# Kernel optimization log

Measured on AMD Instinct MI355X. Metric: run time of the kernel, lower is better.

The kernel has to match this reference:

```python
import jax, jax.numpy as jnp
import numpy as np

B, S, D, H = 2, 2048, 1024, 16
HD = D // H
SCALE = HD ** -0.5

def setup_inputs() -> dict:
    key = jax.random.key(0)
    ks = jax.random.split(key, 5)
    x = jax.random.normal(ks[0], (B, S, D), dtype=jnp.float32)
    Wqkv = jax.random.normal(ks[1], (D, 3 * D), dtype=jnp.float32) * (D ** -0.5)
    bqkv = jnp.zeros((3 * D,), dtype=jnp.float32)
    Wproj = jax.random.normal(ks[2], (D, D), dtype=jnp.float32) * (D ** -0.5)
    bproj = jnp.zeros((D,), dtype=jnp.float32)
    return {"x": x, "Wqkv": Wqkv, "bqkv": bqkv, "Wproj": Wproj, "bproj": bproj}

def reference(x, Wqkv, bqkv, Wproj, bproj):
    b, s, _ = x.shape
    qkv = x @ Wqkv + bqkv                       # [B,S,3D]
    qkv = qkv.reshape(b, s, 3, H, HD)
    q, k, v = [jnp.transpose(qkv[:, :, i], (0, 2, 1, 3)) for i in range(3)]  # [B,H,S,HD]
    attn = jnp.einsum('bhqd,bhkd->bhqk', q, k) * SCALE   # [B,H,S,S]
    attn = jax.nn.softmax(attn, axis=-1)
    out = jnp.einsum('bhqk,bhkd->bhqd', attn, v)         # [B,H,S,HD]
    out = jnp.transpose(out, (0, 2, 1, 3)).reshape(b, s, D)
    return out @ Wproj + bproj
```

## Files before the change

### kernel.cpp

```cpp
#include <hip/hip_runtime.h>
#include <hip/hip_bf16.h>

#define BB 2
#define SS 2048
#define DD 1024
#define HH 16
#define HDD 64
#define MM (BB*SS)
#define NQKV (3*DD)
#define SCALE 0.125f
#define QPRESCALE 0.18033688f

typedef __bf16 bf16_t;
typedef bf16_t bf16x4 __attribute__((ext_vector_type(4)));
typedef bf16_t bf16x8 __attribute__((ext_vector_type(8)));
typedef float f32x4 __attribute__((ext_vector_type(4)));
typedef float f32x16 __attribute__((ext_vector_type(16)));

__device__ __forceinline__ void gl_lds16(const bf16_t* g, bf16_t* l) {
    __builtin_amdgcn_global_load_lds(
        (const __attribute__((address_space(1))) unsigned int*)(uintptr_t)g,
        (__attribute__((address_space(3))) unsigned int*)(uintptr_t)l,
        16, 0, 0);
}

__device__ __forceinline__ f32x4 MF(bf16x8 a, bf16x8 b, f32x4 c) {
    return __builtin_amdgcn_mfma_f32_16x16x32_bf16(a, b, c, 0, 0, 0);
}

__global__ __launch_bounds__(256) void prep(
    const float* __restrict__ x, const float* __restrict__ Wqkv,
    const float* __restrict__ Wproj, bf16_t* __restrict__ xb,
    bf16_t* __restrict__ wqkvt, bf16_t* __restrict__ wprojt)
{
    const int bx = blockIdx.x;
    if (bx < 2048) {
        int i = (bx * 256 + threadIdx.x) * 8;
        float4 a = *(const float4*)(x + i);
        float4 b = *(const float4*)(x + i + 4);
        bf16x8 v;
        v[0]=(bf16_t)a.x; v[1]=(bf16_t)a.y; v[2]=(bf16_t)a.z; v[3]=(bf16_t)a.w;
        v[4]=(bf16_t)b.x; v[5]=(bf16_t)b.y; v[6]=(bf16_t)b.z; v[7]=(bf16_t)b.w;
        *reinterpret_cast<bf16x8*>(xb + i) = v;
        return;
    }
    __shared__ float tile[32][33];
    const float* src; bf16_t* dst; int C, bxl, byl;
    if (bx < 5120) {
        int t = bx - 2048;
        byl = t / 96; bxl = t - byl * 96;
        src = Wqkv;  dst = wqkvt;  C = NQKV;
    } else {
        int t = bx - 5120;
        byl = t >> 5; bxl = t & 31;
        src = Wproj; dst = wprojt; C = DD;
    }
    const int R = DD;
    const int tx = threadIdx.x & 31, ty = threadIdx.x >> 5;
    const int r0 = byl * 32, c0 = bxl * 32;
    #pragma unroll
    for (int i = 0; i < 32; i += 8)
        tile[ty + i][tx] = src[(size_t)(r0 + ty + i) * C + c0 + tx];
    __syncthreads();
    #pragma unroll
    for (int i = 0; i < 32; i += 8)
        dst[(size_t)(c0 + ty + i) * R + r0 + tx] = (bf16_t)tile[tx][ty + i];
}

__global__ __launch_bounds__(512, 2) void gemm_qkv(
    const bf16_t* __restrict__ A, const bf16_t* __restrict__ Bt,
    const float* __restrict__ bias,
    bf16_t* __restrict__ qw, bf16_t* __restrict__ kw, bf16_t* __restrict__ vtw)
{
    constexpr int K  = DD;
    constexpr int BM = 256, BN = 192, BK = 32;
    constexpr int NT = K / BK;

    __shared__ __align__(16) bf16_t smem[50176];
    bf16_t* const Ab[3] = { smem, smem + 8192, smem + 16384 };
    bf16_t* const Bb[3] = { smem + 24576, smem + 30720, smem + 36864 };

    const int tid  = threadIdx.x;
    const int w    = tid >> 6;
    const int lane = tid & 63;
    const int lr   = lane & 15;
    const int quad = lane >> 4;
    const int wm   = w >> 2;
    const int wn   = w & 3;

    const int flat = blockIdx.y * 16 + blockIdx.x;
    const int swz  = (flat & 7) * 32 + (flat >> 3);
    const int m0   = (swz >> 4) * BM;
    const int n0   = (swz & 15) * BN;

    f32x4 acc[8][3];
    #pragma unroll
    for (int mi = 0; mi < 8; mi++)
        #pragma unroll
        for (int ni = 0; ni < 3; ni++)
            acc[mi][ni] = (f32x4){0.f, 0.f, 0.f, 0.f};

    const int ca0 = tid,        ca1 = tid + 512;
    const int cb0 = tid,        cb1 = tid + 256;
    const bf16_t* aG0 = A  + (size_t)(m0 + (ca0 >> 2)) * K + (ca0 & 3) * 8;
    const bf16_t* aG1 = A  + (size_t)(m0 + (ca1 >> 2)) * K + (ca1 & 3) * 8;
    const bf16_t* bG0 = Bt + (size_t)(n0 + (cb0 >> 2)) * K + (cb0 & 3) * 8;
    const bf16_t* bG1 = Bt + (size_t)(n0 + (cb1 >> 2)) * K + (cb1 & 3) * 8;

    auto stage = [&](int kt, bf16_t* Ad, bf16_t* Bd) {
        const int ko = kt * BK;
        gl_lds16(aG0 + ko, Ad + ca0 * 8);
        gl_lds16(aG1 + ko, Ad + ca1 * 8);
        gl_lds16(bG0 + ko, Bd + cb0 * 8);
        gl_lds16(bG1 + ko, Bd + cb1 * 8);
    };

    stage(0, Ab[0], Bb[0]);
    stage(1, Ab[1], Bb[1]);
    asm volatile("s_waitcnt vmcnt(4)" ::: "memory");
    __builtin_amdgcn_s_barrier();
    __builtin_amdgcn_sched_barrier(0);

    const int aOff = (wm * 128 + lr) * BK + quad * 8;
    const int bOff = (wn * 48  + lr) * BK + quad * 8;

    auto tileStep = [&](int t, const bf16_t* Ac, const bf16_t* Bc,
                        bf16_t* An, bf16_t* Bn) {
        bf16x8 af[8], bk[3];
        #pragma unroll
        for (int mi = 0; mi < 8; mi++)
            af[mi] = *(const bf16x8*)(Ac + aOff + mi * 16 * BK);
        #pragma unroll
        for (int ni = 0; ni < 3; ni++)
            bk[ni] = *(const bf16x8*)(Bc + bOff + ni * 16 * BK);
        if (t < NT - 2) stage(t + 2, An, Bn);
        __builtin_amdgcn_sched_barrier(0);
        __builtin_amdgcn_s_setprio(1);
        #pragma unroll
        for (int mi = 0; mi < 8; mi++)
            #pragma unroll
            for (int ni = 0; ni < 3; ni++)
                acc[mi][ni] = MF(af[mi], bk[ni], acc[mi][ni]);
        __builtin_amdgcn_s_setprio(0);
        __builtin_amdgcn_sched_barrier(0);
        if (t < NT - 2)       asm volatile("s_waitcnt vmcnt(4)" ::: "memory");
        else if (t == NT - 2) asm volatile("s_waitcnt vmcnt(0)" ::: "memory");
        __builtin_amdgcn_s_barrier();
        __builtin_amdgcn_sched_barrier(0);
    };

    #pragma unroll 1
    for (int tt = 0; tt < NT - 2; tt += 3) {
        tileStep(tt,     Ab[0], Bb[0], Ab[2], Bb[2]);
        tileStep(tt + 1, Ab[1], Bb[1], Ab[0], Bb[0]);
        tileStep(tt + 2, Ab[2], Bb[2], Ab[1], Bb[1]);
    }
    tileStep(NT - 2, Ab[0], Bb[0], nullptr, nullptr);
    tileStep(NT - 1, Ab[1], Bb[1], nullptr, nullptr);

    __builtin_amdgcn_s_barrier();

    const int colBase = n0 + wn * 48;
    const int vbase   = (n0 < 2048) ? 2048 : n0;
    #pragma unroll
    for (int mi = 0; mi < 8; mi++) {
        const int rl0 = wm * 128 + mi * 16 + quad * 4;
        #pragma unroll
        for (int ni = 0; ni < 3; ni++) {
            const int col = colBase + ni * 16 + lr;
            const float bcol = bias[col];
            const int which = col >> 10;
            const int d = col & 1023;
            const int h = d >> 6, hd = d & 63;
            if (which == 0) {
                #pragma unroll
                for (int reg = 0; reg < 4; reg++) {
                    const int row = m0 + rl0 + reg;
                    const int b = row >> 11, s = row & 2047;
                    qw[(((size_t)(b * HH + h)) * SS + s) * HDD + hd] =
                        (bf16_t)((acc[mi][ni][reg] + bcol) * QPRESCALE);
                }
            } else if (which == 1) {
                #pragma unroll
                for (int reg = 0; reg < 4; reg++) {
                    const int row = m0 + rl0 + reg;
                    const int b = row >> 11, s = row & 2047;
                    kw[(((size_t)(b * HH + h)) * SS + s) * HDD + hd] =
                        (bf16_t)(acc[mi][ni][reg] + bcol);
                }
            } else {
                bf16x4 pk;
                #pragma unroll
                for (int reg = 0; reg < 4; reg++)
                    pk[reg] = (bf16_t)(acc[mi][ni][reg] + bcol);
                const int lc = col - vbase;
                *reinterpret_cast<bf16x4*>(&smem[lc * 260 + rl0]) = pk;
            }
        }
    }
    const int nv = n0 + BN - 2048;
    if (nv > 0) {
        __builtin_amdgcn_s_barrier();
        const int nvc = nv < BN ? nv : BN;
        const int lcb = tid >> 5;
        const int rl  = (tid & 31) * 8;
        const int b   = m0 >> 11;
        const int s   = (m0 & 2047) + rl;
        for (int j = 0; j < nvc / 16; j++) {
            const int lc = j * 16 + lcb;
            bf16x8 vv = *reinterpret_cast<const bf16x8*>(&smem[lc * 260 + rl]);
            const int col = vbase + lc;
            const int d = col & 1023;
            const int h = d >> 6, hd = d & 63;
            *reinterpret_cast<bf16x8*>(
                vtw + (((size_t)(b * HH + h)) * HDD + hd) * SS + s) = vv;
        }
    }
}

__global__ __launch_bounds__(512, 6) void gemm_proj(
    const bf16_t* __restrict__ A, const bf16_t* __restrict__ Bt,
    const float* __restrict__ bias, float* __restrict__ outf)
{
    constexpr int K  = DD;
    constexpr int N  = DD;
    constexpr int BM = 128, BN = 128, BK = 32;
    constexpr int NT = K / BK;

    __shared__ __align__(16) bf16_t smem[24576];
    bf16_t* const Ab[3] = { smem, smem + 4096, smem + 8192 };
    bf16_t* const Bb[3] = { smem + 12288, smem + 16384, smem + 20480 };

    const int tid  = threadIdx.x;
    const int w    = tid >> 6;
    const int lane = tid & 63;
    const int lr   = lane & 15;
    const int quad = lane >> 4;
    const int wm   = w >> 2;
    const int wn   = w & 3;

    const int flat = blockIdx.y * 8 + blockIdx.x;
    const int swz  = (flat & 7) * 32 + (flat >> 3);
    const int m0   = (swz >> 3) * BM;
    const int n0   = (swz & 7) * BN;

    f32x4 acc[4][2];
    #pragma unroll
    for (int mi = 0; mi < 4; mi++)
        #pragma unroll
        for (int ni = 0; ni < 2; ni++)
            acc[mi][ni] = (f32x4){0.f, 0.f, 0.f, 0.f};

    const bf16_t* aG = A  + (size_t)(m0 + (tid >> 2)) * K + (tid & 3) * 8;
    const bf16_t* bG = Bt + (size_t)(n0 + (tid >> 2)) * K + (tid & 3) * 8;

    auto stage = [&](int kt, bf16_t* Ad, bf16_t* Bd) {
        const int ko = kt * BK;
        gl_lds16(aG + ko, Ad + tid * 8);
        gl_lds16(bG + ko, Bd + tid * 8);
    };

    stage(0, Ab[0], Bb[0]);
    stage(1, Ab[1], Bb[1]);
    asm volatile("s_waitcnt vmcnt(2)" ::: "memory");
    __builtin_amdgcn_s_barrier();
    __builtin_amdgcn_sched_barrier(0);

    const int aOff = (wm * 64 + lr) * BK + quad * 8;
    const int bOff = (wn * 32 + lr) * BK + quad * 8;

    auto tileStep = [&](int t, const bf16_t* Ac, const bf16_t* Bc,
                        bf16_t* An, bf16_t* Bn) {
        bf16x8 af[4], bk[2];
        #pragma unroll
        for (int mi = 0; mi < 4; mi++)
            af[mi] = *(const bf16x8*)(Ac + aOff + mi * 16 * BK);
        #pragma unroll
        for (int ni = 0; ni < 2; ni++)
            bk[ni] = *(const bf16x8*)(Bc + bOff + ni * 16 * BK);
        if (t < NT - 2) stage(t + 2, An, Bn);
        __builtin_amdgcn_sched_barrier(0);
        __builtin_amdgcn_s_setprio(1);
        #pragma unroll
        for (int mi = 0; mi < 4; mi++)
            #pragma unroll
            for (int ni = 0; ni < 2; ni++)
                acc[mi][ni] = MF(af[mi], bk[ni], acc[mi][ni]);
        __builtin_amdgcn_s_setprio(0);
        __builtin_amdgcn_sched_barrier(0);
        if (t < NT - 2)       asm volatile("s_waitcnt vmcnt(2)" ::: "memory");
        else if (t == NT - 2) asm volatile("s_waitcnt vmcnt(0)" ::: "memory");
        __builtin_amdgcn_s_barrier();
        __builtin_amdgcn_sched_barrier(0);
    };

    #pragma unroll 1
    for (int tt = 0; tt < NT - 2; tt += 3) {
        tileStep(tt,     Ab[0], Bb[0], Ab[2], Bb[2]);
        tileStep(tt + 1, Ab[1], Bb[1], Ab[0], Bb[0]);
        tileStep(tt + 2, Ab[2], Bb[2], Ab[1], Bb[1]);
    }
    tileStep(NT - 2, Ab[0], Bb[0], nullptr, nullptr);
    tileStep(NT - 1, Ab[1], Bb[1], nullptr, nullptr);

    #pragma unroll
    for (int mi = 0; mi < 4; mi++)
        #pragma unroll
        for (int ni = 0; ni < 2; ni++) {
            const int col = n0 + wn * 32 + ni * 16 + lr;
            const float bcol = bias[col];
            #pragma unroll
            for (int reg = 0; reg < 4; reg++) {
                const int row = m0 + wm * 64 + mi * 16 + quad * 4 + reg;
                outf[(size_t)row * N + col] = acc[mi][ni][reg] + bcol;
            }
        }
}

__global__ __launch_bounds__(512, 4) void attn_kernel(
    const bf16_t* __restrict__ qws, const bf16_t* __restrict__ kws,
    const bf16_t* __restrict__ vtws, bf16_t* __restrict__ ob)
{
    __shared__ __align__(16) bf16_t smem[35072];
    bf16_t* Ks = smem;
    bf16_t* Vs = smem + 16640;

    const int tid  = threadIdx.x;
    const int w    = tid >> 6;
    const int g    = w >> 2;
    const int wg   = w & 3;
    const int lane = tid & 63;
    const int ln31 = lane & 31;
    const int ln5  = lane >> 5;

    const int flat = blockIdx.y * 16 + blockIdx.x;
    const int t2 = flat >> 3;
    const int bh = (t2 >> 4) * 8 + (flat & 7);
    const int qb = t2 & 15;
    const int b  = bh >> 4;
    const int h  = bh & 15;

    const bf16_t* Qh  = qws  + (size_t)bh * SS * HDD;
    const bf16_t* Kh  = kws  + (size_t)bh * SS * HDD;
    const bf16_t* Vth = vtws + (size_t)bh * HDD * SS;

    const int q0w    = qb * 128 + wg * 32;
    const int kvbase = g * 1024;

    bf16x8 aq[4];
    #pragma unroll
    for (int f = 0; f < 4; f++)
        aq[f] = *(const bf16x8*)(Qh + (size_t)(q0w + ln31) * HDD + f * 16 + ln5 * 8);

    const int gtid = tid & 255;
    const int sc = gtid & 7;
    const int sr = gtid >> 3;
    const int vcol = (sc >> 1) * 16 + (sc & 1) * 4;

    {
        const int ko = g * 520;
        const int vo = g * 4608;
        bf16x8 k0 = *(const bf16x8*)(Kh  + (size_t)(kvbase + sr     ) * HDD + sc * 8);
        bf16x8 k1 = *(const bf16x8*)(Kh  + (size_t)(kvbase + sr + 32) * HDD + sc * 8);
        bf16x8 v0 = *(const bf16x8*)(Vth + (size_t)(sr     ) * SS + kvbase + sc * 8);
        bf16x8 v1 = *(const bf16x8*)(Vth + (size_t)(sr + 32) * SS + kvbase + sc * 8);
        *reinterpret_cast<bf16x8*>(&Ks[(ko + sc * 65 + sr     ) * 8]) = k0;
        *reinterpret_cast<bf16x8*>(&Ks[(ko + sc * 65 + sr + 32) * 8]) = k1;
        bf16_t* vd0 = &Vs[vo + (sr     ) * 72 + vcol];
        bf16_t* vd1 = &Vs[vo + (sr + 32) * 72 + vcol];
        *reinterpret_cast<bf16x4*>(vd0)     = __builtin_shufflevector(v0, v0, 0,1,2,3);
        *reinterpret_cast<bf16x4*>(vd0 + 8) = __builtin_shufflevector(v0, v0, 4,5,6,7);
        *reinterpret_cast<bf16x4*>(vd1)     = __builtin_shufflevector(v1, v1, 0,1,2,3);
        *reinterpret_cast<bf16x4*>(vd1 + 8) = __builtin_shufflevector(v1, v1, 4,5,6,7);
    }
    __syncthreads();

    float l = 0.f;
    f32x16 o[2];
    #pragma unroll
    for (int nh = 0; nh < 2; nh++)
        #pragma unroll
        for (int r = 0; r < 16; r++) o[nh][r] = 0.f;

    int buf = 0;
    for (int it = 0; it < 16; ++it) {
        const int ko = buf * 1040 + g * 520;
        const int vo = buf * 9216 + g * 4608;

        bf16x8 nk0, nk1, nv0, nv1;
        const bool more = (it + 1 < 16);
        if (more) {
            const int kvn = kvbase + (it + 1) * 64;
            nk0 = *(const bf16x8*)(Kh  + (size_t)(kvn + sr     ) * HDD + sc * 8);
            nk1 = *(const bf16x8*)(Kh  + (size_t)(kvn + sr + 32) * HDD + sc * 8);
            nv0 = *(const bf16x8*)(Vth + (size_t)(sr     ) * SS + kvn + sc * 8);
            nv1 = *(const bf16x8*)(Vth + (size_t)(sr + 32) * SS + kvn + sc * 8);
        }

        f32x16 sfr[2];
        __builtin_amdgcn_s_setprio(1);
        #pragma unroll
        for (int ni = 0; ni < 2; ni++) {
            #pragma unroll
            for (int r = 0; r < 16; r++) sfr[ni][r] = 0.f;
            #pragma unroll
            for (int f = 0; f < 4; f++) {
                bf16x8 kb = *reinterpret_cast<const bf16x8*>(
                    &Ks[(ko + (2 * f + ln5) * 65 + ni * 32 + ln31) * 8]);
                sfr[ni] = __builtin_amdgcn_mfma_f32_32x32x16_bf16(kb, aq[f], sfr[ni], 0, 0, 0);
            }
        }
        __builtin_amdgcn_s_setprio(0);

        float p[2][16];
        #pragma unroll
        for (int ni = 0; ni < 2; ni++)
            #pragma unroll
            for (int r = 0; r < 16; r++) {
                p[ni][r] = __builtin_amdgcn_exp2f(sfr[ni][r]);
                l += p[ni][r];
            }

        bf16x8 ap[4];
        #pragma unroll
        for (int c16 = 0; c16 < 4; c16++)
            #pragma unroll
            for (int j = 0; j < 8; j++)
                ap[c16][j] = (bf16_t)p[c16 >> 1][(c16 & 1) * 8 + j];

        __builtin_amdgcn_s_setprio(1);
        #pragma unroll
        for (int nh = 0; nh < 2; nh++) {
            const bf16_t* vrow = &Vs[vo + (nh * 32 + ln31) * 72];
            #pragma unroll
            for (int c16 = 0; c16 < 4; c16++) {
                bf16x8 vb = *reinterpret_cast<const bf16x8*>(vrow + c16 * 16 + 8 * ln5);
                o[nh] = __builtin_amdgcn_mfma_f32_32x32x16_bf16(ap[c16], vb, o[nh], 0, 0, 0);
            }
        }
        __builtin_amdgcn_s_setprio(0);

        if (more) {
            const int ko1 = (buf ^ 1) * 1040 + g * 520;
            const int vo1 = (buf ^ 1) * 9216 + g * 4608;
            *reinterpret_cast<bf16x8*>(&Ks[(ko1 + sc * 65 + sr     ) * 8]) = nk0;
            *reinterpret_cast<bf16x8*>(&Ks[(ko1 + sc * 65 + sr + 32) * 8]) = nk1;
            bf16_t* vd0 = &Vs[vo1 + (sr     ) * 72 + vcol];
            bf16_t* vd1 = &Vs[vo1 + (sr + 32) * 72 + vcol];
            *reinterpret_cast<bf16x4*>(vd0)     = __builtin_shufflevector(nv0, nv0, 0,1,2,3);
            *reinterpret_cast<bf16x4*>(vd0 + 8) = __builtin_shufflevector(nv0, nv0, 4,5,6,7);
            *reinterpret_cast<bf16x4*>(vd1)     = __builtin_shufflevector(nv1, nv1, 0,1,2,3);
            *reinterpret_cast<bf16x4*>(vd1 + 8) = __builtin_shufflevector(nv1, nv1, 4,5,6,7);
        }
        __syncthreads();
        buf ^= 1;
    }

    l += __shfl_xor(l, 32, 64);

    __syncthreads();
    float* Of = (float*)smem;
    float* Lf = (float*)(smem + 16384);
    if (ln5 == 0) Lf[g * 128 + wg * 32 + ln31] = l;
    if (g == 1) {
        #pragma unroll
        for (int nh = 0; nh < 2; nh++)
            #pragma unroll
            for (int r = 0; r < 16; r++) {
                const int q = (r & 3) + 8 * (r >> 2) + 4 * ln5;
                Of[(wg * 32 + q) * 64 + nh * 32 + ln31] = o[nh][r];
            }
    }
    __syncthreads();
    if (g == 0) {
        float inv[16];
        #pragma unroll
        for (int r = 0; r < 16; r++) {
            const int q = (r & 3) + 8 * (r >> 2) + 4 * ln5;
            inv[r] = 1.f / (Lf[wg * 32 + q] + Lf[128 + wg * 32 + q]);
        }
        #pragma unroll
        for (int nh = 0; nh < 2; nh++)
            #pragma unroll
            for (int r = 0; r < 16; r++) {
                const int q  = (r & 3) + 8 * (r >> 2) + 4 * ln5;
                const int hd = nh * 32 + ln31;
                float val = (o[nh][r] + Of[(wg * 32 + q) * 64 + hd]) * inv[r];
                ob[((size_t)b * SS + q0w + q) * DD + h * HDD + hd] = (bf16_t)val;
            }
    }
}

extern "C" void kernel_launch(void* const* d_in, const int* in_sizes, int n_in,
                              void* d_out, int out_size, void* d_ws, size_t ws_size,
                              hipStream_t stream) {
    const float* x     = (const float*)d_in[0];
    const float* Wqkv  = (const float*)d_in[1];
    const float* bqkv  = (const float*)d_in[2];
    const float* Wproj = (const float*)d_in[3];
    const float* bproj = (const float*)d_in[4];
    float* out = (float*)d_out;

    const size_t NEL = (size_t)MM * DD;
    bf16_t* qws    = (bf16_t*)d_ws;
    bf16_t* kws    = qws  + NEL;
    bf16_t* vtws   = kws  + NEL;
    bf16_t* xb     = vtws + NEL;
    bf16_t* ows    = xb;
    bf16_t* wqkvt  = xb + NEL;
    bf16_t* wprojt = wqkvt + (size_t)NQKV * DD;

    prep<<<6144, 256, 0, stream>>>(x, Wqkv, Wproj, xb, wqkvt, wprojt);

    gemm_qkv<<<dim3(NQKV / 192, MM / 256), 512, 0, stream>>>(
        xb, wqkvt, bqkv, qws, kws, vtws);

    attn_kernel<<<dim3(SS / 128, BB * HH), 512, 0, stream>>>(qws, kws, vtws, ows);

    gemm_proj<<<dim3(DD / 128, MM / 128), 512, 0, stream>>>(
        ows, wprojt, bproj, out);
}
```

Baseline: 172.3 us.

## Shrink QKV GEMM tiles to 128x128 with XCD-aware block mapping

The QKV projection GEMM moves from 256x192 tiles at 2 blocks/CU to 128x128 tiles at up to 6 blocks/CU, which gives 768 blocks instead of 256. A new XCD-aware swizzle assigns each XCD a contiguous region of M and N tiles for L2 reuse. Because each tile now lies entirely in Q, K or V, the epilogue picks its destination once per block instead of per column. The smaller tiles raise occupancy and wave balance across CUs but lower per-block operand reuse and increase global traffic.

```diff
diff --git a/kernel.cpp b/kernel.cpp
--- a/kernel.cpp
+++ b/kernel.cpp
@@ -67,18 +67,18 @@
         dst[(size_t)(c0 + ty + i) * R + r0 + tx] = (bf16_t)tile[tx][ty + i];
 }
 
-__global__ __launch_bounds__(512, 2) void gemm_qkv(
+__global__ __launch_bounds__(512, 6) void gemm_qkv(
     const bf16_t* __restrict__ A, const bf16_t* __restrict__ Bt,
     const float* __restrict__ bias,
     bf16_t* __restrict__ qw, bf16_t* __restrict__ kw, bf16_t* __restrict__ vtw)
 {
     constexpr int K  = DD;
-    constexpr int BM = 256, BN = 192, BK = 32;
+    constexpr int BM = 128, BN = 128, BK = 32;
     constexpr int NT = K / BK;
 
-    __shared__ __align__(16) bf16_t smem[50176];
-    bf16_t* const Ab[3] = { smem, smem + 8192, smem + 16384 };
-    bf16_t* const Bb[3] = { smem + 24576, smem + 30720, smem + 36864 };
+    __shared__ __align__(16) bf16_t smem[24576];
+    bf16_t* const Ab[3] = { smem,         smem + 4096,  smem + 8192 };
+    bf16_t* const Bb[3] = { smem + 12288, smem + 16384, smem + 20480 };
 
     const int tid  = threadIdx.x;
     const int w    = tid >> 6;
@@ -88,62 +88,57 @@
     const int wm   = w >> 2;
     const int wn   = w & 3;
 
-    const int flat = blockIdx.y * 16 + blockIdx.x;
-    const int swz  = (flat & 7) * 32 + (flat >> 3);
-    const int m0   = (swz >> 4) * BM;
-    const int n0   = (swz & 15) * BN;
-
-    f32x4 acc[8][3];
-    #pragma unroll
-    for (int mi = 0; mi < 8; mi++)
-        #pragma unroll
-        for (int ni = 0; ni < 3; ni++)
+    const int flat = blockIdx.y * 24 + blockIdx.x;
+    const int xcd  = flat & 7;
+    const int idx  = flat >> 3;
+    const int m0   = ((xcd >> 1) * 8 + (idx & 7)) * BM;
+    const int n0   = ((xcd & 1) * 12 + (idx >> 3)) * BN;
+
+    f32x4 acc[4][2];
+    #pragma unroll
+    for (int mi = 0; mi < 4; mi++)
+        #pragma unroll
+        for (int ni = 0; ni < 2; ni++)
             acc[mi][ni] = (f32x4){0.f, 0.f, 0.f, 0.f};
 
-    const int ca0 = tid,        ca1 = tid + 512;
-    const int cb0 = tid,        cb1 = tid + 256;
-    const bf16_t* aG0 = A  + (size_t)(m0 + (ca0 >> 2)) * K + (ca0 & 3) * 8;
-    const bf16_t* aG1 = A  + (size_t)(m0 + (ca1 >> 2)) * K + (ca1 & 3) * 8;
-    const bf16_t* bG0 = Bt + (size_t)(n0 + (cb0 >> 2)) * K + (cb0 & 3) * 8;
-    const bf16_t* bG1 = Bt + (size_t)(n0 + (cb1 >> 2)) * K + (cb1 & 3) * 8;
+    const bf16_t* aG = A  + (size_t)(m0 + (tid >> 2)) * K + (tid & 3) * 8;
+    const bf16_t* bG = Bt + (size_t)(n0 + (tid >> 2)) * K + (tid & 3) * 8;
 
     auto stage = [&](int kt, bf16_t* Ad, bf16_t* Bd) {
         const int ko = kt * BK;
-        gl_lds16(aG0 + ko, Ad + ca0 * 8);
-        gl_lds16(aG1 + ko, Ad + ca1 * 8);
-        gl_lds16(bG0 + ko, Bd + cb0 * 8);
-        gl_lds16(bG1 + ko, Bd + cb1 * 8);
+        gl_lds16(aG + ko, Ad + tid * 8);
+        gl_lds16(bG + ko, Bd + tid * 8);
     };
 
     stage(0, Ab[0], Bb[0]);
     stage(1, Ab[1], Bb[1]);
-    asm volatile("s_waitcnt vmcnt(4)" ::: "memory");
+    asm volatile("s_waitcnt vmcnt(2)" ::: "memory");
     __builtin_amdgcn_s_barrier();
     __builtin_amdgcn_sched_barrier(0);
 
-    const int aOff = (wm * 128 + lr) * BK + quad * 8;
-    const int bOff = (wn * 48  + lr) * BK + quad * 8;
+    const int aOff = (wm * 64 + lr) * BK + quad * 8;
+    const int bOff = (wn * 32 + lr) * BK + quad * 8;
 
     auto tileStep = [&](int t, const bf16_t* Ac, const bf16_t* Bc,
                         bf16_t* An, bf16_t* Bn) {
-        bf16x8 af[8], bk[3];
-        #pragma unroll
-        for (int mi = 0; mi < 8; mi++)
+        bf16x8 af[4], bk[2];
+        #pragma unroll
+        for (int mi = 0; mi < 4; mi++)
             af[mi] = *(const bf16x8*)(Ac + aOff + mi * 16 * BK);
         #pragma unroll
-        for (int ni = 0; ni < 3; ni++)
+        for (int ni = 0; ni < 2; ni++)
             bk[ni] = *(const bf16x8*)(Bc + bOff + ni * 16 * BK);
         if (t < NT - 2) stage(t + 2, An, Bn);
         __builtin_amdgcn_sched_barrier(0);
         __builtin_amdgcn_s_setprio(1);
         #pragma unroll
-        for (int mi = 0; mi < 8; mi++)
-            #pragma unroll
-            for (int ni = 0; ni < 3; ni++)
+        for (int mi = 0; mi < 4; mi++)
+            #pragma unroll
+            for (int ni = 0; ni < 2; ni++)
                 acc[mi][ni] = MF(af[mi], bk[ni], acc[mi][ni]);
         __builtin_amdgcn_s_setprio(0);
         __builtin_amdgcn_sched_barrier(0);
-        if (t < NT - 2)       asm volatile("s_waitcnt vmcnt(4)" ::: "memory");
+        if (t < NT - 2)       asm volatile("s_waitcnt vmcnt(2)" ::: "memory");
         else if (t == NT - 2) asm volatile("s_waitcnt vmcnt(0)" ::: "memory");
         __builtin_amdgcn_s_barrier();
         __builtin_amdgcn_sched_barrier(0);
@@ -158,59 +153,56 @@
     tileStep(NT - 2, Ab[0], Bb[0], nullptr, nullptr);
     tileStep(NT - 1, Ab[1], Bb[1], nullptr, nullptr);
 
-    __builtin_amdgcn_s_barrier();
-
-    const int colBase = n0 + wn * 48;
-    const int vbase   = (n0 < 2048) ? 2048 : n0;
-    #pragma unroll
-    for (int mi = 0; mi < 8; mi++) {
-        const int rl0 = wm * 128 + mi * 16 + quad * 4;
-        #pragma unroll
-        for (int ni = 0; ni < 3; ni++) {
-            const int col = colBase + ni * 16 + lr;
-            const float bcol = bias[col];
-            const int which = col >> 10;
-            const int d = col & 1023;
-            const int h = d >> 6, hd = d & 63;
-            if (which == 0) {
+    const int which = n0 >> 10;
+    const int dbase = n0 & 1023;
+    const int b     = m0 >> 11;
+    const int s0    = m0 & 2047;
+
+    if (which < 2) {
+        bf16_t* dst = (which == 0) ? qw : kw;
+        const float scale = (which == 0) ? QPRESCALE : 1.0f;
+        #pragma unroll
+        for (int mi = 0; mi < 4; mi++) {
+            const int rl0 = wm * 64 + mi * 16 + quad * 4;
+            #pragma unroll
+            for (int ni = 0; ni < 2; ni++) {
+                const int col = n0 + wn * 32 + ni * 16 + lr;
+                const float bcol = bias[col];
+                const int d = col & 1023;
+                const int h = d >> 6, hd = d & 63;
                 #pragma unroll
                 for (int reg = 0; reg < 4; reg++) {
-                    const int row = m0 + rl0 + reg;
-                    const int b = row >> 11, s = row & 2047;
-                    qw[(((size_t)(b * HH + h)) * SS + s) * HDD + hd] =
-                        (bf16_t)((acc[mi][ni][reg] + bcol) * QPRESCALE);
+                    const int s = s0 + rl0 + reg;
+                    dst[(((size_t)(b * HH + h)) * SS + s) * HDD + hd] =
+                        (bf16_t)((acc[mi][ni][reg] + bcol) * scale);
                 }
-            } else if (which == 1) {
-                #pragma unroll
-                for (int reg = 0; reg < 4; reg++) {
-                    const int row = m0 + rl0 + reg;
-                    const int b = row >> 11, s = row & 2047;
-                    kw[(((size_t)(b * HH + h)) * SS + s) * HDD + hd] =
-                        (bf16_t)(acc[mi][ni][reg] + bcol);
-                }
-            } else {
+            }
+        }
+    } else {
+        __builtin_amdgcn_s_barrier();
+        #pragma unroll
+        for (int mi = 0; mi < 4; mi++) {
+            const int rl0 = wm * 64 + mi * 16 + quad * 4;
+            #pragma unroll
+            for (int ni = 0; ni < 2; ni++) {
+                const int lc = wn * 32 + ni * 16 + lr;
+                const float bcol = bias[n0 + lc];
                 bf16x4 pk;
                 #pragma unroll
                 for (int reg = 0; reg < 4; reg++)
                     pk[reg] = (bf16_t)(acc[mi][ni][reg] + bcol);
-                const int lc = col - vbase;
-                *reinterpret_cast<bf16x4*>(&smem[lc * 260 + rl0]) = pk;
-            }
-        }
-    }
-    const int nv = n0 + BN - 2048;
-    if (nv > 0) {
+                *reinterpret_cast<bf16x4*>(&smem[lc * 132 + rl0]) = pk;
+            }
+        }
         __builtin_amdgcn_s_barrier();
-        const int nvc = nv < BN ? nv : BN;
-        const int lcb = tid >> 5;
-        const int rl  = (tid & 31) * 8;
-        const int b   = m0 >> 11;
-        const int s   = (m0 & 2047) + rl;
-        for (int j = 0; j < nvc / 16; j++) {
-            const int lc = j * 16 + lcb;
-            bf16x8 vv = *reinterpret_cast<const bf16x8*>(&smem[lc * 260 + rl]);
-            const int col = vbase + lc;
-            const int d = col & 1023;
+        const int lcb = tid >> 4;
+        const int rl  = (tid & 15) * 8;
+        const int s   = s0 + rl;
+        #pragma unroll
+        for (int j = 0; j < 4; j++) {
+            const int lc = j * 32 + lcb;
+            bf16x8 vv = *reinterpret_cast<const bf16x8*>(&smem[lc * 132 + rl]);
+            const int d = dbase + lc;
             const int h = d >> 6, hd = d & 63;
             *reinterpret_cast<bf16x8*>(
                 vtw + (((size_t)(b * HH + h)) * HDD + hd) * SS + s) = vv;
@@ -512,7 +504,7 @@
 
     prep<<<6144, 256, 0, stream>>>(x, Wqkv, Wproj, xb, wqkvt, wprojt);
 
-    gemm_qkv<<<dim3(NQKV / 192, MM / 256), 512, 0, stream>>>(
+    gemm_qkv<<<dim3(NQKV / 128, MM / 128), 512, 0, stream>>>(
         xb, wqkvt, bqkv, qws, kws, vtws);
 
     attn_kernel<<<dim3(SS / 128, BB * HH), 512, 0, stream>>>(qws, kws, vtws, ows);
```

Result: no change. 174.3 us, median of 2 (+1.1%).
